# Optimization experiments

Hardware: AMD Instinct MI355X
Metric: run time of the kernel (lower is better)

## Reference

```python
import jax, jax.numpy as jnp
import numpy as np

N_NODES, N_LINKS, N_PATHS = 512, 4096, 20000
D = 128        # node_state_dim == path_state_dim
HEADS = 24
R = 256        # readout units
T_STEPS = 3    # config['t']
MAX_LEN = 8


def _gru(x, h, W, U, b):
    # Keras GRUCell (reset_after=True), gate order [z, r, h]
    xg = x @ W + b[0]
    hg = h @ U + b[1]
    xz, xr, xh = jnp.split(xg, 3, axis=-1)
    hz, hr, hh = jnp.split(hg, 3, axis=-1)
    z = jax.nn.sigmoid(xz + hz)
    r = jax.nn.sigmoid(xr + hr)
    hc = jnp.tanh(xh + r * hh)
    return z * h + (1.0 - z) * hc


def _masked_gru(x_seq, mask, h0, W, U, b, reverse):
    # x_seq [P,T,D], mask [P,T]; Keras masked RNN semantics:
    # state copies through masked steps, output copies previous output (init 0)
    if reverse:
        x_seq = x_seq[:, ::-1]
        mask = mask[:, ::-1]
    def step(carry, inp):
        h, o = carry
        x_t, m_t = inp
        h_new = _gru(x_t, h, W, U, b)
        m = m_t[:, None]
        h = jnp.where(m, h_new, h)
        o = jnp.where(m, h_new, o)
        return (h, o), o
    (hT, _), outs = jax.lax.scan(step, (h0, jnp.zeros_like(h0)),
                                 (x_seq.transpose(1, 0, 2), mask.T))
    outs = outs.transpose(1, 0, 2)
    if reverse:
        outs = outs[:, ::-1]
    return outs, hT


def _gat(x, adj, W, a_self, a_neigh, bias):
    # spektral-style dense GraphAttention, concat_heads=False (mean over heads)
    xp = jnp.einsum('nf,fhc->nhc', x, W)                 # [N,H,C]
    e_s = jnp.einsum('nhc,hc->nh', xp, a_self)
    e_n = jnp.einsum('nhc,hc->nh', xp, a_neigh)
    logits = e_s.T[:, :, None] + e_n.T[:, None, :]       # [H,N,N]
    logits = jax.nn.leaky_relu(logits, 0.2)
    logits = jnp.where(adj[None] == 0.0, -1e9, logits)
    attn = jax.nn.softmax(logits, axis=-1)
    return jnp.einsum('hij,jhc->ihc', attn, xp).mean(axis=1) + bias


def setup_inputs() -> dict:
    rng = np.random.default_rng(0)
    lens = rng.integers(4, MAX_LEN + 1, size=N_PATHS)
    paths = np.repeat(np.arange(N_PATHS, dtype=np.int32), lens)
    seqs = np.concatenate([np.arange(l, dtype=np.int32) for l in lens])
    nodes = rng.integers(0, N_NODES, size=paths.shape[0]).astype(np.int32)
    adj_idx = rng.choice(N_NODES * N_NODES, size=N_LINKS, replace=False).astype(np.int32)

    key = jax.random.key(0)
    ks = iter(jax.random.split(key, 40))
    nrm = lambda *s: jax.random.normal(next(ks), s, dtype=jnp.float32) * 0.05
    unif = lambda *s: jax.random.uniform(next(ks), s, dtype=jnp.float32)
    return {
        'ToS': unif(N_PATHS), 'bandwith': unif(N_PATHS),
        'q_policy': jnp.asarray(rng.integers(0, 3, N_NODES), jnp.float32),
        'w1': unif(N_NODES), 'w2': unif(N_NODES), 'w3': unif(N_NODES),
        'queue_size': unif(N_NODES, 3), 'link_capacity': unif(N_LINKS),
        'gat_W': nrm(D, HEADS, D), 'gat_as': nrm(HEADS, D), 'gat_an': nrm(HEADS, D),
        'gat_b': jnp.zeros((D,), jnp.float32),
        'Wp': nrm(D, 3 * D), 'Up': nrm(D, 3 * D), 'bp': jnp.zeros((2, 3 * D), jnp.float32),
        'Wb': nrm(D, 3 * D), 'Ub': nrm(D, 3 * D), 'bb': jnp.zeros((2, 3 * D), jnp.float32),
        'Wn': nrm(D, 3 * D), 'Un': nrm(D, 3 * D), 'bn': jnp.zeros((2, 3 * D), jnp.float32),
        'rW1': nrm(D, R), 'rb1': jnp.zeros((R,), jnp.float32),
        'rW2': nrm(R, R), 'rb2': jnp.zeros((R,), jnp.float32),
        'rW3': nrm(R, 1), 'rb3': jnp.zeros((1,), jnp.float32),
        'paths': jnp.asarray(paths), 'seqs': jnp.asarray(seqs),
        'nodes': jnp.asarray(nodes), 'adj_idx': jnp.asarray(adj_idx),
    }


def reference(ToS, bandwith, q_policy, w1, w2, w3, queue_size, link_capacity,
              gat_W, gat_as, gat_an, gat_b, Wp, Up, bp, Wb, Ub, bb, Wn, Un, bn,
              rW1, rb1, rW2, rb2, rW3, rb3, paths, seqs, nodes, adj_idx):
    node_state = jnp.concatenate([q_policy[:, None], w1[:, None], w2[:, None],
                                  w3[:, None], queue_size,
                                  jnp.zeros((N_NODES, D - 7), jnp.float32)], axis=1)
    path_state = jnp.concatenate([bandwith[:, None], ToS[:, None],
                                  jnp.zeros((N_PATHS, D - 2), jnp.float32)], axis=1)
    adj = jnp.zeros(N_NODES * N_NODES, jnp.float32).at[adj_idx].set(link_capacity)
    adj = adj.reshape(N_NODES, N_NODES)
    adj = adj / jnp.sqrt(jnp.sum(adj * adj))  # tf.linalg.normalize (global L2)

    lens = jax.ops.segment_sum(jnp.ones_like(paths), paths, num_segments=N_PATHS)
    mask = jnp.arange(MAX_LEN)[None, :] < lens[:, None]  # [P,T]

    for _ in range(T_STEPS):
        node_state = _gat(node_state, adj, gat_W, gat_as, gat_an, gat_b)
        h_tild = node_state[nodes]  # [S,D]
        node_inputs = jnp.zeros((N_PATHS, MAX_LEN, D), jnp.float32).at[paths, seqs].set(h_tild)
        out_f, h_f = _masked_gru(node_inputs, mask, path_state, Wp, Up, bp, False)
        out_b, _ = _masked_gru(node_inputs, mask, path_state, Wb, Ub, bb, True)
        outputs = out_f + out_b  # Bidirectional merge_mode='sum'
        path_state = h_f
        m2 = outputs[paths, seqs]
        m2 = jax.ops.segment_sum(m2, nodes, num_segments=N_NODES)
        node_state = _gru(m2, node_state, Wn, Un, bn)

    h = jax.nn.selu(path_state @ rW1 + rb1)
    h = jax.nn.relu(h @ rW2 + rb2)
    return h @ rW3 + rb3
```

## Files before the change

### kernel.cpp

```cpp
#include <hip/hip_runtime.h>
#include <math.h>

#define NN 512
#define NP 20000
#define DD 128
#define NH 24
#define G3 384
#define NHD 3072

typedef __attribute__((ext_vector_type(8))) short bf8_t;
typedef __attribute__((ext_vector_type(4))) float f4_t;
typedef unsigned short ushort_t;

__device__ __forceinline__ float sigf(float x){
  return __builtin_amdgcn_rcpf(1.f + __expf(-x));
}
__device__ __forceinline__ float tanh_fast(float x){
  float ax = fabsf(x);
  float e = __expf(-2.f*ax);
  float t = (1.f - e) * __builtin_amdgcn_rcpf(1.f + e);
  return copysignf(t, x);
}
__device__ __forceinline__ unsigned short f2bf(float f){
  unsigned int u = __float_as_uint(f);
  unsigned int r = (u + 0x7fffu + ((u>>16)&1u)) >> 16;
  return (unsigned short)r;
}
__device__ __forceinline__ float bf2f(unsigned short h){
  return __uint_as_float(((unsigned int)h)<<16);
}

__global__ void k_init_ns(float* ns, const float* qp, const float* w1, const float* w2,
                          const float* w3, const float* qs){
  int n = blockIdx.x, c = threadIdx.x;
  float v = 0.f;
  if (c==0) v=qp[n]; else if (c==1) v=w1[n]; else if (c==2) v=w2[n]; else if (c==3) v=w3[n];
  else if (c<7) v=qs[n*3 + (c-4)];
  ns[n*DD+c]=v;
}

__global__ void k_init_ps(float* ps, const float* bw, const float* tos){
  int i = blockIdx.x*256 + threadIdx.x;
  if (i >= NP*DD) return;
  int p = i>>7, c = i&127;
  float v=0.f; if(c==0) v=bw[p]; else if(c==1) v=tos[p];
  ps[i]=v;
}

__global__ void k_adj(unsigned int* adjb, const int* idx, const float* lc){
  int l = blockIdx.x*256+threadIdx.x; if(l>=4096) return;
  if (lc[l]!=0.f){
    int a = idx[l]; int i = a>>9, j = a&511;
    atomicOr(&adjb[i*16 + (j>>5)], 1u<<(j&31));
  }
}

__global__ void k_meta(const int* paths, const int* seqs, int* start, int* lens, int E){
  int e = blockIdx.x*256+threadIdx.x; if(e>=E) return;
  int p=paths[e], s=seqs[e];
  if (s==0) start[p]=e;
  if (e==E-1 || paths[e+1]!=p) lens[p]=s+1;
}

__global__ void k_lcount(const int* __restrict__ lens, int* lcnt){
  int p = blockIdx.x*256+threadIdx.x; if(p>=NP) return;
  atomicAdd(&lcnt[lens[p]],1);
}
__global__ void k_lscan(const int* __restrict__ lcnt, int* loff, int* lcur){
  if (threadIdx.x==0){
    int acc=0;
    for (int L=15; L>=0; --L){ loff[L]=acc; lcur[L]=acc; acc+=lcnt[L]; }
  }
}
__global__ void k_lfill(const int* __restrict__ lens, int* lcur, int* perm){
  int p = blockIdx.x*256+threadIdx.x; if(p>=NP) return;
  int pos = atomicAdd(&lcur[lens[p]],1);
  perm[pos]=p;
}

__global__ void k_wsplit(const float* __restrict__ W, ushort_t* __restrict__ Wh,
                         ushort_t* __restrict__ Wl, int shift, int ncols, int total){
  int i = blockIdx.x*256 + threadIdx.x;
  if (i >= total) return;
  int col = i >> shift, k = i & ((1<<shift)-1);
  float v = W[(size_t)k*ncols + col];
  ushort_t h = f2bf(v);
  Wh[i] = h; Wl[i] = f2bf(v - bf2f(h));
}

__global__ __launch_bounds__(512) void k_xp2(const float* __restrict__ ns,
                      const ushort_t* __restrict__ gwh, const ushort_t* __restrict__ gwl,
                      float* __restrict__ xp){
  __shared__ __align__(16) ushort_t XsH[32][136], XsL[32][136];
  int r0 = blockIdx.x*32, c0 = blockIdx.y*256;
  int tid = threadIdx.x;
  int w = tid>>6, l = tid&63, lr = l&15, lg = l>>4;
  for (int idx=tid; idx<32*128; idx+=512){
    int pp=idx>>7, kk=idx&127;
    float v = ns[(size_t)(r0+pp)*DD+kk];
    ushort_t hi=f2bf(v); XsH[pp][kk]=hi; XsL[pp][kk]=f2bf(v-bf2f(hi));
  }
  __syncthreads();
  int col0 = c0 + w*32 + lr, col1 = col0 + 16;
  f4_t a00=(f4_t)(0.f), a01=(f4_t)(0.f), a10=(f4_t)(0.f), a11=(f4_t)(0.f);
  #pragma unroll
  for (int kt=0; kt<4; kt++){
    int kof = kt*32 + lg*8;
    const bf8_t Ah0 = *(const bf8_t*)&XsH[lr][kof];
    const bf8_t Al0 = *(const bf8_t*)&XsL[lr][kof];
    const bf8_t Ah1 = *(const bf8_t*)&XsH[16+lr][kof];
    const bf8_t Al1 = *(const bf8_t*)&XsL[16+lr][kof];
    const bf8_t B0h = *(const bf8_t*)(gwh + (size_t)col0*128 + kof);
    const bf8_t B0l = *(const bf8_t*)(gwl + (size_t)col0*128 + kof);
    const bf8_t B1h = *(const bf8_t*)(gwh + (size_t)col1*128 + kof);
    const bf8_t B1l = *(const bf8_t*)(gwl + (size_t)col1*128 + kof);
    a00 = __builtin_amdgcn_mfma_f32_16x16x32_bf16(Ah0,B0h,a00,0,0,0);
    a00 = __builtin_amdgcn_mfma_f32_16x16x32_bf16(Al0,B0h,a00,0,0,0);
    a00 = __builtin_amdgcn_mfma_f32_16x16x32_bf16(Ah0,B0l,a00,0,0,0);
    a01 = __builtin_amdgcn_mfma_f32_16x16x32_bf16(Ah0,B1h,a01,0,0,0);
    a01 = __builtin_amdgcn_mfma_f32_16x16x32_bf16(Al0,B1h,a01,0,0,0);
    a01 = __builtin_amdgcn_mfma_f32_16x16x32_bf16(Ah0,B1l,a01,0,0,0);
    a10 = __builtin_amdgcn_mfma_f32_16x16x32_bf16(Ah1,B0h,a10,0,0,0);
    a10 = __builtin_amdgcn_mfma_f32_16x16x32_bf16(Al1,B0h,a10,0,0,0);
    a10 = __builtin_amdgcn_mfma_f32_16x16x32_bf16(Ah1,B0l,a10,0,0,0);
    a11 = __builtin_amdgcn_mfma_f32_16x16x32_bf16(Ah1,B1h,a11,0,0,0);
    a11 = __builtin_amdgcn_mfma_f32_16x16x32_bf16(Al1,B1h,a11,0,0,0);
    a11 = __builtin_amdgcn_mfma_f32_16x16x32_bf16(Ah1,B1l,a11,0,0,0);
  }
  #pragma unroll
  for (int q=0;q<4;q++){
    int row0 = lg*4+q, row1 = 16+lg*4+q;
    xp[(size_t)(r0+row0)*NHD + col0] = a00[q];
    xp[(size_t)(r0+row0)*NHD + col1] = a01[q];
    xp[(size_t)(r0+row1)*NHD + col0] = a10[q];
    xp[(size_t)(r0+row1)*NHD + col1] = a11[q];
  }
}

__global__ __launch_bounds__(256) void k_gat_e2(const float* __restrict__ xp,
                        const float* __restrict__ as_, const float* __restrict__ an_,
                        float* es, float* en){
  int n = blockIdx.x; int tid = threadIdx.x;
  int w = tid>>6, l = tid&63;
  for (int hh=0; hh<6; hh++){
    int h = w*6 + hh;
    const float* xr = xp + ((size_t)n*NH + h)*DD;
    const float* ar = as_ + h*DD; const float* br = an_ + h*DD;
    float s1 = xr[l]*ar[l] + xr[l+64]*ar[l+64];
    float s2 = xr[l]*br[l] + xr[l+64]*br[l+64];
    for (int o=32;o>0;o>>=1){ s1 += __shfl_down(s1,o); s2 += __shfl_down(s2,o); }
    if (l==0){ es[n*NH+h]=s1; en[n*NH+h]=s2; }
  }
}

__global__ __launch_bounds__(256) void k_attn(const float* __restrict__ xp,
                      const float* __restrict__ es, const float* __restrict__ en,
                      const unsigned int* __restrict__ adjb, float* __restrict__ pbuf){
  __shared__ float lg[32][513];
  __shared__ float mxs[32], isms[32];
  int h = blockIdx.x, it = blockIdx.y; int i0 = it*32; int tid = threadIdx.x;
  for (int idx=tid; idx<32*512; idx+=256){
    int ii = idx>>9, j = idx&511;
    float l = es[(i0+ii)*NH+h] + en[j*NH+h];
    l = (l>=0.f)? l : 0.2f*l;
    unsigned int m = adjb[(i0+ii)*16 + (j>>5)];
    if (!((m>>(j&31))&1u)) l = -1000000000.0f;
    lg[ii][j] = l;
  }
  __syncthreads();
  {
    int t8 = tid&7, ii = tid>>3;
    float m = -INFINITY;
    for (int j=t8;j<512;j+=8) m = fmaxf(m, lg[ii][j]);
    for (int o=4;o>0;o>>=1) m = fmaxf(m, __shfl_xor(m, o));
    float s=0.f;
    for (int j=t8;j<512;j+=8) s += __expf(lg[ii][j]-m);
    for (int o=4;o>0;o>>=1) s += __shfl_xor(s,o);
    if (t8==0){ mxs[ii]=m; isms[ii]=__builtin_amdgcn_rcpf(s); }
  }
  __syncthreads();
  for (int idx=tid; idx<32*512; idx+=256){
    int ii = idx>>9, j = idx&511;
    lg[ii][j] = __expf(lg[ii][j]-mxs[ii])*isms[ii];
  }
  __syncthreads();
  int cq = tid&31, iq = tid>>5; int c = cq*4;
  float4 acc0=make_float4(0,0,0,0), acc1=acc0, acc2=acc0, acc3=acc0;
  for (int j=0;j<512;j++){
    const float4 xv = *(const float4*)(xp + ((size_t)j*NH + h)*DD + c);
    float p0 = lg[iq*4+0][j], p1 = lg[iq*4+1][j], p2 = lg[iq*4+2][j], p3 = lg[iq*4+3][j];
    acc0.x+=p0*xv.x; acc0.y+=p0*xv.y; acc0.z+=p0*xv.z; acc0.w+=p0*xv.w;
    acc1.x+=p1*xv.x; acc1.y+=p1*xv.y; acc1.z+=p1*xv.z; acc1.w+=p1*xv.w;
    acc2.x+=p2*xv.x; acc2.y+=p2*xv.y; acc2.z+=p2*xv.z; acc2.w+=p2*xv.w;
    acc3.x+=p3*xv.x; acc3.y+=p3*xv.y; acc3.z+=p3*xv.z; acc3.w+=p3*xv.w;
  }
  *(float4*)(pbuf + (((size_t)h*NN + i0+iq*4+0)*DD) + c) = acc0;
  *(float4*)(pbuf + (((size_t)h*NN + i0+iq*4+1)*DD) + c) = acc1;
  *(float4*)(pbuf + (((size_t)h*NN + i0+iq*4+2)*DD) + c) = acc2;
  *(float4*)(pbuf + (((size_t)h*NN + i0+iq*4+3)*DD) + c) = acc3;
}

__global__ void k_gred(const float* __restrict__ pbuf, const float* __restrict__ gb,
                       float* __restrict__ gout){
  int n = blockIdx.x, c = threadIdx.x;
  float a = 0.f;
  #pragma unroll
  for (int h=0; h<NH; h++) a += pbuf[((size_t)h*NN + n)*DD + c];
  gout[n*DD+c] = a*(1.f/24.f) + gb[c];
}

__global__ __launch_bounds__(512) void k_xg3(const float* __restrict__ gout,
      const ushort_t* __restrict__ WpH, const ushort_t* __restrict__ WpL,
      const ushort_t* __restrict__ WbH, const ushort_t* __restrict__ WbL,
      const float* __restrict__ bpF, const float* __restrict__ bpB,
      float* __restrict__ xgF, float* __restrict__ xgB){
  __shared__ __align__(16) ushort_t XsH[32][136], XsL[32][136];
  int r0 = blockIdx.x*32;
  int mat = blockIdx.y/3, cg = blockIdx.y%3;
  const ushort_t* Wh = mat? WbH : WpH;
  const ushort_t* Wl = mat? WbL : WpL;
  const float* b0 = mat? bpB : bpF;
  float* out = mat? xgB : xgF;
  int tid = threadIdx.x;
  int w = tid>>6, l = tid&63, lr = l&15, lg = l>>4;
  for (int idx=tid; idx<32*128; idx+=512){
    int pp=idx>>7, kk=idx&127;
    float v = gout[(size_t)(r0+pp)*DD+kk];
    ushort_t hi=f2bf(v); XsH[pp][kk]=hi; XsL[pp][kk]=f2bf(v-bf2f(hi));
  }
  __syncthreads();
  int col = cg*128 + w*16 + lr;
  f4_t a0=(f4_t)(0.f), a1=(f4_t)(0.f);
  #pragma unroll
  for (int kt=0; kt<4; kt++){
    int kof = kt*32 + lg*8;
    const bf8_t Ah0 = *(const bf8_t*)&XsH[lr][kof];
    const bf8_t Al0 = *(const bf8_t*)&XsL[lr][kof];
    const bf8_t Ah1 = *(const bf8_t*)&XsH[16+lr][kof];
    const bf8_t Al1 = *(const bf8_t*)&XsL[16+lr][kof];
    const bf8_t Bh = *(const bf8_t*)(Wh + (size_t)col*128 + kof);
    const bf8_t Bl = *(const bf8_t*)(Wl + (size_t)col*128 + kof);
    a0 = __builtin_amdgcn_mfma_f32_16x16x32_bf16(Ah0,Bh,a0,0,0,0);
    a0 = __builtin_amdgcn_mfma_f32_16x16x32_bf16(Al0,Bh,a0,0,0,0);
    a0 = __builtin_amdgcn_mfma_f32_16x16x32_bf16(Ah0,Bl,a0,0,0,0);
    a1 = __builtin_amdgcn_mfma_f32_16x16x32_bf16(Ah1,Bh,a1,0,0,0);
    a1 = __builtin_amdgcn_mfma_f32_16x16x32_bf16(Al1,Bh,a1,0,0,0);
    a1 = __builtin_amdgcn_mfma_f32_16x16x32_bf16(Ah1,Bl,a1,0,0,0);
  }
  float bb0 = b0[col];
  #pragma unroll
  for (int q=0;q<4;q++){
    out[(size_t)(r0+lg*4+q)*G3 + col]    = a0[q] + bb0;
    out[(size_t)(r0+16+lg*4+q)*G3 + col] = a1[q] + bb0;
  }
}

__global__ __launch_bounds__(512) void k_gru2(
    const float* __restrict__ ps_in, float* __restrict__ ps_out,
    const float* __restrict__ xgF, const float* __restrict__ xgB,
    const ushort_t* __restrict__ UthF, const ushort_t* __restrict__ UtlF,
    const ushort_t* __restrict__ UthB, const ushort_t* __restrict__ UtlB,
    const float* __restrict__ b1F, const float* __restrict__ b1B,
    const int* __restrict__ start, const int* __restrict__ lens,
    const int* __restrict__ nodes, const int* __restrict__ perm,
    float* __restrict__ m2)
{
  __shared__ __align__(16) ushort_t HsH[2][32][136];
  __shared__ __align__(16) ushort_t HsL[2][32][136];
  __shared__ int Ls[32], Ss[32], Pid[32];
  __shared__ int nid_l[32][8];

  int dir = blockIdx.x & 1, pblk = blockIdx.x >> 1;
  const bool rev = (dir==1);
  const float* xg = rev ? xgB : xgF;
  const ushort_t* Uth = rev ? UthB : UthF;
  const ushort_t* Utl = rev ? UtlB : UtlF;
  const float* b1 = rev ? b1B : b1F;
  float* psn = rev ? (float*)0 : ps_out;

  int pb = pblk*32;
  int tid = threadIdx.x;
  int w = tid>>6, l = tid&63;
  int lr = l&15, lg = l>>4;
  int c = w*16 + lr;

  if (tid<32){ int pid = perm[pb+tid]; Pid[tid]=pid; Ls[tid]=lens[pid]; Ss[tid]=start[pid]; }
  __syncthreads();
  for (int idx=tid; idx<32*128; idx+=512){
    int pp=idx>>7, kk=idx&127;
    float v = ps_in[(size_t)Pid[pp]*DD+kk];
    ushort_t hi = f2bf(v);
    HsH[0][pp][kk]=hi; HsL[0][pp][kk]=f2bf(v - bf2f(hi));
  }
  if (tid<256){
    int p=tid>>3, s=tid&7; int L=Ls[p];
    int nid = 0;
    if (s<L){ int pos = rev ? (L-1-s) : s; nid = nodes[Ss[p]+pos]; }
    nid_l[p][s]=nid;
  }
  __syncthreads();

  int Lmax = Ls[0];
  int Lv[8];
  #pragma unroll
  for (int i=0;i<8;i++){ int p=(i>>2)*16 + lg*4 + (i&3); Lv[i]=Ls[p]; }
  float b1z = b1[c], b1r = b1[128+c], b1h = b1[256+c];

  int cur = 0;
  for (int s=0;s<Lmax;s++){
    int nxt = cur^1;
    bool act[8]; int niv[8]; float xzv[8], xrv[8], xhv[8];
    #pragma unroll
    for (int i=0;i<8;i++){
      int p=(i>>2)*16 + lg*4 + (i&3);
      act[i] = (s < Lv[i]);
      int nid = nid_l[p][s];
      niv[i] = nid;
      const float* xr = xg + (size_t)nid*G3;
      xzv[i]=xr[c]; xrv[i]=xr[128+c]; xhv[i]=xr[256+c];
    }
    f4_t accz0=(f4_t)(0.f), accz1=(f4_t)(0.f);
    f4_t accr0=(f4_t)(0.f), accr1=(f4_t)(0.f);
    f4_t acch0=(f4_t)(0.f), acch1=(f4_t)(0.f);
    #pragma unroll
    for (int kt=0; kt<4; kt++){
      int kof = kt*32 + lg*8;
      const bf8_t Ahi0 = *(const bf8_t*)&HsH[cur][lr][kof];
      const bf8_t Alo0 = *(const bf8_t*)&HsL[cur][lr][kof];
      const bf8_t Ahi1 = *(const bf8_t*)&HsH[cur][16+lr][kof];
      const bf8_t Alo1 = *(const bf8_t*)&HsL[cur][16+lr][kof];
      const bf8_t Bhz = *(const bf8_t*)(Uth + ((size_t)(      c))*128 + kof);
      const bf8_t Blz = *(const bf8_t*)(Utl + ((size_t)(      c))*128 + kof);
      const bf8_t Bhr = *(const bf8_t*)(Uth + ((size_t)(128 + c))*128 + kof);
      const bf8_t Blr = *(const bf8_t*)(Utl + ((size_t)(128 + c))*128 + kof);
      const bf8_t Bhh = *(const bf8_t*)(Uth + ((size_t)(256 + c))*128 + kof);
      const bf8_t Blh = *(const bf8_t*)(Utl + ((size_t)(256 + c))*128 + kof);
      accz0 = __builtin_amdgcn_mfma_f32_16x16x32_bf16(Ahi0, Bhz, accz0, 0,0,0);
      accz0 = __builtin_amdgcn_mfma_f32_16x16x32_bf16(Alo0, Bhz, accz0, 0,0,0);
      accz0 = __builtin_amdgcn_mfma_f32_16x16x32_bf16(Ahi0, Blz, accz0, 0,0,0);
      accz1 = __builtin_amdgcn_mfma_f32_16x16x32_bf16(Ahi1, Bhz, accz1, 0,0,0);
      accz1 = __builtin_amdgcn_mfma_f32_16x16x32_bf16(Alo1, Bhz, accz1, 0,0,0);
      accz1 = __builtin_amdgcn_mfma_f32_16x16x32_bf16(Ahi1, Blz, accz1, 0,0,0);
      accr0 = __builtin_amdgcn_mfma_f32_16x16x32_bf16(Ahi0, Bhr, accr0, 0,0,0);
      accr0 = __builtin_amdgcn_mfma_f32_16x16x32_bf16(Alo0, Bhr, accr0, 0,0,0);
      accr0 = __builtin_amdgcn_mfma_f32_16x16x32_bf16(Ahi0, Blr, accr0, 0,0,0);
      accr1 = __builtin_amdgcn_mfma_f32_16x16x32_bf16(Ahi1, Bhr, accr1, 0,0,0);
      accr1 = __builtin_amdgcn_mfma_f32_16x16x32_bf16(Alo1, Bhr, accr1, 0,0,0);
      accr1 = __builtin_amdgcn_mfma_f32_16x16x32_bf16(Ahi1, Blr, accr1, 0,0,0);
      acch0 = __builtin_amdgcn_mfma_f32_16x16x32_bf16(Ahi0, Bhh, acch0, 0,0,0);
      acch0 = __builtin_amdgcn_mfma_f32_16x16x32_bf16(Alo0, Bhh, acch0, 0,0,0);
      acch0 = __builtin_amdgcn_mfma_f32_16x16x32_bf16(Ahi0, Blh, acch0, 0,0,0);
      acch1 = __builtin_amdgcn_mfma_f32_16x16x32_bf16(Ahi1, Bhh, acch1, 0,0,0);
      acch1 = __builtin_amdgcn_mfma_f32_16x16x32_bf16(Alo1, Bhh, acch1, 0,0,0);
      acch1 = __builtin_amdgcn_mfma_f32_16x16x32_bf16(Ahi1, Blh, acch1, 0,0,0);
    }
#define EPI(i, mt, qq, AZ, AR, AH) { \
    int p = (mt)*16 + lg*4 + (qq); \
    if (act[i]) { \
      float hold = bf2f(HsH[cur][p][c]) + bf2f(HsL[cur][p][c]); \
      float z = sigf(xzv[i] + (AZ) + b1z); \
      float r = sigf(xrv[i] + (AR) + b1r); \
      float hc = tanh_fast(xhv[i] + r*((AH) + b1h)); \
      float hn = z*hold + (1.f-z)*hc; \
      ushort_t hi2 = f2bf(hn); \
      HsH[nxt][p][c]=hi2; HsL[nxt][p][c]=f2bf(hn - bf2f(hi2)); \
      atomicAdd(&m2[(size_t)niv[i]*DD + c], hn); \
    } else { \
      HsH[nxt][p][c]=HsH[cur][p][c]; HsL[nxt][p][c]=HsL[cur][p][c]; \
    } }
    EPI(0,0,0, accz0.x, accr0.x, acch0.x)
    EPI(1,0,1, accz0.y, accr0.y, acch0.y)
    EPI(2,0,2, accz0.z, accr0.z, acch0.z)
    EPI(3,0,3, accz0.w, accr0.w, acch0.w)
    EPI(4,1,0, accz1.x, accr1.x, acch1.x)
    EPI(5,1,1, accz1.y, accr1.y, acch1.y)
    EPI(6,1,2, accz1.z, accr1.z, acch1.z)
    EPI(7,1,3, accz1.w, accr1.w, acch1.w)
#undef EPI
    __syncthreads();
    cur = nxt;
  }
  if (psn){
    for (int idx=tid; idx<32*128; idx+=512){
      int pp=idx>>7, kk=idx&127;
      psn[(size_t)Pid[pp]*DD+kk] = bf2f(HsH[cur][pp][kk]) + bf2f(HsL[cur][pp][kk]);
    }
  }
}

__global__ __launch_bounds__(512) void k_ngru3(
    const float* __restrict__ m2, const float* __restrict__ gout,
    const ushort_t* __restrict__ WnH, const ushort_t* __restrict__ WnL,
    const ushort_t* __restrict__ UnH, const ushort_t* __restrict__ UnL,
    const float* __restrict__ bn, float* __restrict__ ns)
{
  __shared__ __align__(16) ushort_t MsH[32][136], MsL[32][136];
  __shared__ __align__(16) ushort_t GsH[32][136], GsL[32][136];
  int r0 = blockIdx.x*32;
  int tid = threadIdx.x;
  int w = tid>>6, l = tid&63, lr = l&15, lg = l>>4;
  for (int idx=tid; idx<32*128; idx+=512){
    int pp=idx>>7, kk=idx&127;
    float vm = m2[(size_t)(r0+pp)*DD+kk];
    float vg = gout[(size_t)(r0+pp)*DD+kk];
    ushort_t hm=f2bf(vm); MsH[pp][kk]=hm; MsL[pp][kk]=f2bf(vm-bf2f(hm));
    ushort_t hg=f2bf(vg); GsH[pp][kk]=hg; GsL[pp][kk]=f2bf(vg-bf2f(hg));
  }
  __syncthreads();
  int c = w*16 + lr;
  f4_t xz0=(f4_t)(0.f), xr0=(f4_t)(0.f), xh0=(f4_t)(0.f);
  f4_t xz1=(f4_t)(0.f), xr1=(f4_t)(0.f), xh1=(f4_t)(0.f);
  f4_t hz0=(f4_t)(0.f), hr0=(f4_t)(0.f), hh0=(f4_t)(0.f);
  f4_t hz1=(f4_t)(0.f), hr1=(f4_t)(0.f), hh1=(f4_t)(0.f);
  #pragma unroll
  for (int kt=0; kt<4; kt++){
    int kof = kt*32 + lg*8;
    const bf8_t MA0h = *(const bf8_t*)&MsH[lr][kof];
    const bf8_t MA0l = *(const bf8_t*)&MsL[lr][kof];
    const bf8_t MA1h = *(const bf8_t*)&MsH[16+lr][kof];
    const bf8_t MA1l = *(const bf8_t*)&MsL[16+lr][kof];
    const bf8_t GA0h = *(const bf8_t*)&GsH[lr][kof];
    const bf8_t GA0l = *(const bf8_t*)&GsL[lr][kof];
    const bf8_t GA1h = *(const bf8_t*)&GsH[16+lr][kof];
    const bf8_t GA1l = *(const bf8_t*)&GsL[16+lr][kof];
    const bf8_t Wzh = *(const bf8_t*)(WnH + ((size_t)(      c))*128 + kof);
    const bf8_t Wzl = *(const bf8_t*)(WnL + ((size_t)(      c))*128 + kof);
    const bf8_t Wrh = *(const bf8_t*)(WnH + ((size_t)(128 + c))*128 + kof);
    const bf8_t Wrl = *(const bf8_t*)(WnL + ((size_t)(128 + c))*128 + kof);
    const bf8_t Whh = *(const bf8_t*)(WnH + ((size_t)(256 + c))*128 + kof);
    const bf8_t Whl = *(const bf8_t*)(WnL + ((size_t)(256 + c))*128 + kof);
    const bf8_t Uzh = *(const bf8_t*)(UnH + ((size_t)(      c))*128 + kof);
    const bf8_t Uzl = *(const bf8_t*)(UnL + ((size_t)(      c))*128 + kof);
    const bf8_t Urh = *(const bf8_t*)(UnH + ((size_t)(128 + c))*128 + kof);
    const bf8_t Url = *(const bf8_t*)(UnL + ((size_t)(128 + c))*128 + kof);
    const bf8_t Uhh = *(const bf8_t*)(UnH + ((size_t)(256 + c))*128 + kof);
    const bf8_t Uhl = *(const bf8_t*)(UnL + ((size_t)(256 + c))*128 + kof);
    xz0 = __builtin_amdgcn_mfma_f32_16x16x32_bf16(MA0h,Wzh,xz0,0,0,0);
    xz0 = __builtin_amdgcn_mfma_f32_16x16x32_bf16(MA0l,Wzh,xz0,0,0,0);
    xz0 = __builtin_amdgcn_mfma_f32_16x16x32_bf16(MA0h,Wzl,xz0,0,0,0);
    xz1 = __builtin_amdgcn_mfma_f32_16x16x32_bf16(MA1h,Wzh,xz1,0,0,0);
    xz1 = __builtin_amdgcn_mfma_f32_16x16x32_bf16(MA1l,Wzh,xz1,0,0,0);
    xz1 = __builtin_amdgcn_mfma_f32_16x16x32_bf16(MA1h,Wzl,xz1,0,0,0);
    xr0 = __builtin_amdgcn_mfma_f32_16x16x32_bf16(MA0h,Wrh,xr0,0,0,0);
    xr0 = __builtin_amdgcn_mfma_f32_16x16x32_bf16(MA0l,Wrh,xr0,0,0,0);
    xr0 = __builtin_amdgcn_mfma_f32_16x16x32_bf16(MA0h,Wrl,xr0,0,0,0);
    xr1 = __builtin_amdgcn_mfma_f32_16x16x32_bf16(MA1h,Wrh,xr1,0,0,0);
    xr1 = __builtin_amdgcn_mfma_f32_16x16x32_bf16(MA1l,Wrh,xr1,0,0,0);
    xr1 = __builtin_amdgcn_mfma_f32_16x16x32_bf16(MA1h,Wrl,xr1,0,0,0);
    xh0 = __builtin_amdgcn_mfma_f32_16x16x32_bf16(MA0h,Whh,xh0,0,0,0);
    xh0 = __builtin_amdgcn_mfma_f32_16x16x32_bf16(MA0l,Whh,xh0,0,0,0);
    xh0 = __builtin_amdgcn_mfma_f32_16x16x32_bf16(MA0h,Whl,xh0,0,0,0);
    xh1 = __builtin_amdgcn_mfma_f32_16x16x32_bf16(MA1h,Whh,xh1,0,0,0);
    xh1 = __builtin_amdgcn_mfma_f32_16x16x32_bf16(MA1l,Whh,xh1,0,0,0);
    xh1 = __builtin_amdgcn_mfma_f32_16x16x32_bf16(MA1h,Whl,xh1,0,0,0);
    hz0 = __builtin_amdgcn_mfma_f32_16x16x32_bf16(GA0h,Uzh,hz0,0,0,0);
    hz0 = __builtin_amdgcn_mfma_f32_16x16x32_bf16(GA0l,Uzh,hz0,0,0,0);
    hz0 = __builtin_amdgcn_mfma_f32_16x16x32_bf16(GA0h,Uzl,hz0,0,0,0);
    hz1 = __builtin_amdgcn_mfma_f32_16x16x32_bf16(GA1h,Uzh,hz1,0,0,0);
    hz1 = __builtin_amdgcn_mfma_f32_16x16x32_bf16(GA1l,Uzh,hz1,0,0,0);
    hz1 = __builtin_amdgcn_mfma_f32_16x16x32_bf16(GA1h,Uzl,hz1,0,0,0);
    hr0 = __builtin_amdgcn_mfma_f32_16x16x32_bf16(GA0h,Urh,hr0,0,0,0);
    hr0 = __builtin_amdgcn_mfma_f32_16x16x32_bf16(GA0l,Urh,hr0,0,0,0);
    hr0 = __builtin_amdgcn_mfma_f32_16x16x32_bf16(GA0h,Url,hr0,0,0,0);
    hr1 = __builtin_amdgcn_mfma_f32_16x16x32_bf16(GA1h,Urh,hr1,0,0,0);
    hr1 = __builtin_amdgcn_mfma_f32_16x16x32_bf16(GA1l,Urh,hr1,0,0,0);
    hr1 = __builtin_amdgcn_mfma_f32_16x16x32_bf16(GA1h,Url,hr1,0,0,0);
    hh0 = __builtin_amdgcn_mfma_f32_16x16x32_bf16(GA0h,Uhh,hh0,0,0,0);
    hh0 = __builtin_amdgcn_mfma_f32_16x16x32_bf16(GA0l,Uhh,hh0,0,0,0);
    hh0 = __builtin_amdgcn_mfma_f32_16x16x32_bf16(GA0h,Uhl,hh0,0,0,0);
    hh1 = __builtin_amdgcn_mfma_f32_16x16x32_bf16(GA1h,Uhh,hh1,0,0,0);
    hh1 = __builtin_amdgcn_mfma_f32_16x16x32_bf16(GA1l,Uhh,hh1,0,0,0);
    hh1 = __builtin_amdgcn_mfma_f32_16x16x32_bf16(GA1h,Uhl,hh1,0,0,0);
  }
  float bz = bn[c] + bn[G3+c], br = bn[128+c] + bn[G3+128+c];
  float bxh = bn[256+c], bhh = bn[G3+256+c];
  #pragma unroll
  for (int q=0;q<4;q++){
    {
      int n = lg*4+q;
      float hval = bf2f(GsH[n][c]) + bf2f(GsL[n][c]);
      float z = sigf(xz0[q] + hz0[q] + bz);
      float r = sigf(xr0[q] + hr0[q] + br);
      float hc = tanh_fast(xh0[q] + bxh + r*(hh0[q] + bhh));
      ns[(size_t)(r0+n)*DD + c] = z*hval + (1.f-z)*hc;
    }
    {
      int n = 16+lg*4+q;
      float hval = bf2f(GsH[n][c]) + bf2f(GsL[n][c]);
      float z = sigf(xz1[q] + hz1[q] + bz);
      float r = sigf(xr1[q] + hr1[q] + br);
      float hc = tanh_fast(xh1[q] + bxh + r*(hh1[q] + bhh));
      ns[(size_t)(r0+n)*DD + c] = z*hval + (1.f-z)*hc;
    }
  }
}

__global__ __launch_bounds__(512) void k_read2(
    const float* __restrict__ ps,
    const ushort_t* __restrict__ r1h, const ushort_t* __restrict__ r1l,
    const ushort_t* __restrict__ r2h, const ushort_t* __restrict__ r2l,
    const float* __restrict__ rb1, const float* __restrict__ rb2,
    const float* __restrict__ rW3, const float* __restrict__ rb3,
    float* __restrict__ out)
{
  __shared__ __align__(16) ushort_t XsH[32][136], XsL[32][136];
  __shared__ __align__(16) char buf[32*264*2*2];
  ushort_t (*H1H)[264] = (ushort_t(*)[264])buf;
  ushort_t (*H1L)[264] = (ushort_t(*)[264])(buf + 32*264*2);
  float (*H2)[257] = (float(*)[257])buf;
  int pb = blockIdx.x*32, tid = threadIdx.x;
  int w = tid>>6, l = tid&63, lr = l&15, lg = l>>4;
  for (int idx=tid; idx<32*128; idx+=512){
    int pp=idx>>7, kk=idx&127;
    float v = ps[(size_t)(pb+pp)*DD+kk];
    ushort_t hi=f2bf(v); XsH[pp][kk]=hi; XsL[pp][kk]=f2bf(v-bf2f(hi));
  }
  __syncthreads();
  int col0 = w*32 + lr, col1 = col0 + 16;
  f4_t a00=(f4_t)(0.f), a01=(f4_t)(0.f), a10=(f4_t)(0.f), a11=(f4_t)(0.f);
  #pragma unroll
  for (int kt=0; kt<4; kt++){
    int kof = kt*32 + lg*8;
    const bf8_t Ah0 = *(const bf8_t*)&XsH[lr][kof];
    const bf8_t Al0 = *(const bf8_t*)&XsL[lr][kof];
    const bf8_t Ah1 = *(const bf8_t*)&XsH[16+lr][kof];
    const bf8_t Al1 = *(const bf8_t*)&XsL[16+lr][kof];
    const bf8_t B0h = *(const bf8_t*)(r1h + (size_t)col0*128 + kof);
    const bf8_t B0l = *(const bf8_t*)(r1l + (size_t)col0*128 + kof);
    const bf8_t B1h = *(const bf8_t*)(r1h + (size_t)col1*128 + kof);
    const bf8_t B1l = *(const bf8_t*)(r1l + (size_t)col1*128 + kof);
    a00 = __builtin_amdgcn_mfma_f32_16x16x32_bf16(Ah0,B0h,a00,0,0,0);
    a00 = __builtin_amdgcn_mfma_f32_16x16x32_bf16(Al0,B0h,a00,0,0,0);
    a00 = __builtin_amdgcn_mfma_f32_16x16x32_bf16(Ah0,B0l,a00,0,0,0);
    a01 = __builtin_amdgcn_mfma_f32_16x16x32_bf16(Ah0,B1h,a01,0,0,0);
    a01 = __builtin_amdgcn_mfma_f32_16x16x32_bf16(Al0,B1h,a01,0,0,0);
    a01 = __builtin_amdgcn_mfma_f32_16x16x32_bf16(Ah0,B1l,a01,0,0,0);
    a10 = __builtin_amdgcn_mfma_f32_16x16x32_bf16(Ah1,B0h,a10,0,0,0);
    a10 = __builtin_amdgcn_mfma_f32_16x16x32_bf16(Al1,B0h,a10,0,0,0);
    a10 = __builtin_amdgcn_mfma_f32_16x16x32_bf16(Ah1,B0l,a10,0,0,0);
    a11 = __builtin_amdgcn_mfma_f32_16x16x32_bf16(Ah1,B1h,a11,0,0,0);
    a11 = __builtin_amdgcn_mfma_f32_16x16x32_bf16(Al1,B1h,a11,0,0,0);
    a11 = __builtin_amdgcn_mfma_f32_16x16x32_bf16(Ah1,B1l,a11,0,0,0);
  }
  float rb1c0 = rb1[col0], rb1c1 = rb1[col1];
  #pragma unroll
  for (int q=0;q<4;q++){
    int row0 = lg*4+q, row1 = 16+lg*4+q;
    float v00 = a00[q]+rb1c0, v01 = a01[q]+rb1c1, v10 = a10[q]+rb1c0, v11 = a11[q]+rb1c1;
    v00 = 1.0507009873554805f * (v00>0.f ? v00 : 1.6732632423543772f*(__expf(v00)-1.f));
    v01 = 1.0507009873554805f * (v01>0.f ? v01 : 1.6732632423543772f*(__expf(v01)-1.f));
    v10 = 1.0507009873554805f * (v10>0.f ? v10 : 1.6732632423543772f*(__expf(v10)-1.f));
    v11 = 1.0507009873554805f * (v11>0.f ? v11 : 1.6732632423543772f*(__expf(v11)-1.f));
    ushort_t h;
    h=f2bf(v00); H1H[row0][col0]=h; H1L[row0][col0]=f2bf(v00-bf2f(h));
    h=f2bf(v01); H1H[row0][col1]=h; H1L[row0][col1]=f2bf(v01-bf2f(h));
    h=f2bf(v10); H1H[row1][col0]=h; H1L[row1][col0]=f2bf(v10-bf2f(h));
    h=f2bf(v11); H1H[row1][col1]=h; H1L[row1][col1]=f2bf(v11-bf2f(h));
  }
  __syncthreads();
  f4_t c00=(f4_t)(0.f), c01=(f4_t)(0.f), c10=(f4_t)(0.f), c11=(f4_t)(0.f);
  #pragma unroll
  for (int kt=0; kt<8; kt++){
    int kof = kt*32 + lg*8;
    const bf8_t Ah0 = *(const bf8_t*)&H1H[lr][kof];
    const bf8_t Al0 = *(const bf8_t*)&H1L[lr][kof];
    const bf8_t Ah1 = *(const bf8_t*)&H1H[16+lr][kof];
    const bf8_t Al1 = *(const bf8_t*)&H1L[16+lr][kof];
    const bf8_t B0h = *(const bf8_t*)(r2h + (size_t)col0*256 + kof);
    const bf8_t B0l = *(const bf8_t*)(r2l + (size_t)col0*256 + kof);
    const bf8_t B1h = *(const bf8_t*)(r2h + (size_t)col1*256 + kof);
    const bf8_t B1l = *(const bf8_t*)(r2l + (size_t)col1*256 + kof);
    c00 = __builtin_amdgcn_mfma_f32_16x16x32_bf16(Ah0,B0h,c00,0,0,0);
    c00 = __builtin_amdgcn_mfma_f32_16x16x32_bf16(Al0,B0h,c00,0,0,0);
    c00 = __builtin_amdgcn_mfma_f32_16x16x32_bf16(Ah0,B0l,c00,0,0,0);
    c01 = __builtin_amdgcn_mfma_f32_16x16x32_bf16(Ah0,B1h,c01,0,0,0);
    c01 = __builtin_amdgcn_mfma_f32_16x16x32_bf16(Al0,B1h,c01,0,0,0);
    c01 = __builtin_amdgcn_mfma_f32_16x16x32_bf16(Ah0,B1l,c01,0,0,0);
    c10 = __builtin_amdgcn_mfma_f32_16x16x32_bf16(Ah1,B0h,c10,0,0,0);
    c10 = __builtin_amdgcn_mfma_f32_16x16x32_bf16(Al1,B0h,c10,0,0,0);
    c10 = __builtin_amdgcn_mfma_f32_16x16x32_bf16(Ah1,B0l,c10,0,0,0);
    c11 = __builtin_amdgcn_mfma_f32_16x16x32_bf16(Ah1,B1h,c11,0,0,0);
    c11 = __builtin_amdgcn_mfma_f32_16x16x32_bf16(Al1,B1h,c11,0,0,0);
    c11 = __builtin_amdgcn_mfma_f32_16x16x32_bf16(Ah1,B1l,c11,0,0,0);
  }
  __syncthreads();
  float rb2c0 = rb2[col0], rb2c1 = rb2[col1];
  #pragma unroll
  for (int q=0;q<4;q++){
    int row0 = lg*4+q, row1 = 16+lg*4+q;
    H2[row0][col0] = fmaxf(c00[q]+rb2c0, 0.f);
    H2[row0][col1] = fmaxf(c01[q]+rb2c1, 0.f);
    H2[row1][col0] = fmaxf(c10[q]+rb2c0, 0.f);
    H2[row1][col1] = fmaxf(c11[q]+rb2c1, 0.f);
  }
  __syncthreads();
  int r = tid>>4, j0 = tid&15;
  float s = 0.f;
  for (int j=j0; j<256; j+=16) s += H2[r][j]*rW3[j];
  for (int o=8;o>0;o>>=1) s += __shfl_xor(s,o);
  if (j0==0) out[pb+r] = s + rb3[0];
}

extern "C" void kernel_launch(void* const* d_in, const int* in_sizes, int n_in,
                              void* d_out, int out_size, void* d_ws, size_t ws_size,
                              hipStream_t stream)
{
  const float* ToS   = (const float*)d_in[0];
  const float* bw    = (const float*)d_in[1];
  const float* qpol  = (const float*)d_in[2];
  const float* w1    = (const float*)d_in[3];
  const float* w2    = (const float*)d_in[4];
  const float* w3    = (const float*)d_in[5];
  const float* qs    = (const float*)d_in[6];
  const float* lc    = (const float*)d_in[7];
  const float* gat_W = (const float*)d_in[8];
  const float* gat_as= (const float*)d_in[9];
  const float* gat_an= (const float*)d_in[10];
  const float* gat_b = (const float*)d_in[11];
  const float* Wp    = (const float*)d_in[12];
  const float* Up    = (const float*)d_in[13];
  const float* bp    = (const float*)d_in[14];
  const float* Wb    = (const float*)d_in[15];
  const float* Ub    = (const float*)d_in[16];
  const float* bb    = (const float*)d_in[17];
  const float* Wn    = (const float*)d_in[18];
  const float* Un    = (const float*)d_in[19];
  const float* bn    = (const float*)d_in[20];
  const float* rW1   = (const float*)d_in[21];
  const float* rb1   = (const float*)d_in[22];
  const float* rW2   = (const float*)d_in[23];
  const float* rb2   = (const float*)d_in[24];
  const float* rW3   = (const float*)d_in[25];
  const float* rb3   = (const float*)d_in[26];
  const int* paths   = (const int*)d_in[27];
  const int* seqs    = (const int*)d_in[28];
  const int* nodes   = (const int*)d_in[29];
  const int* adj_idx = (const int*)d_in[30];
  int E = in_sizes[27];

  char* w0 = (char*)d_ws;
  char* w = w0;
  auto alloc = [&](size_t nbytes)->void*{ void* r=(void*)w; w += (nbytes + 255) & ~(size_t)255; return r; };
  float* ns     = (float*)alloc((size_t)NN*DD*4);
  float* gout   = (float*)alloc((size_t)NN*DD*4);
  float* psA    = (float*)alloc((size_t)NP*DD*4);
  float* psB    = (float*)alloc((size_t)NP*DD*4);
  float* xp     = (float*)alloc((size_t)NN*NHD*4);
  float* es     = (float*)alloc((size_t)NN*NH*4);
  float* en     = (float*)alloc((size_t)NN*NH*4);
  unsigned int* adjb = (unsigned int*)alloc((size_t)NN*16*4);
  float* xgp    = (float*)alloc((size_t)NN*G3*4);
  float* xgb    = (float*)alloc((size_t)NN*G3*4);
  float* m2     = (float*)alloc((size_t)NN*DD*4);
  float* pbuf   = (float*)alloc((size_t)NH*NN*DD*4);
  ushort_t* Uthp = (ushort_t*)alloc((size_t)G3*DD*2);
  ushort_t* Utlp = (ushort_t*)alloc((size_t)G3*DD*2);
  ushort_t* Uthb = (ushort_t*)alloc((size_t)G3*DD*2);
  ushort_t* Utlb = (ushort_t*)alloc((size_t)G3*DD*2);
  ushort_t* Wpth = (ushort_t*)alloc((size_t)G3*DD*2);
  ushort_t* Wptl = (ushort_t*)alloc((size_t)G3*DD*2);
  ushort_t* Wbth = (ushort_t*)alloc((size_t)G3*DD*2);
  ushort_t* Wbtl = (ushort_t*)alloc((size_t)G3*DD*2);
  ushort_t* WnTh = (ushort_t*)alloc((size_t)G3*DD*2);
  ushort_t* WnTl = (ushort_t*)alloc((size_t)G3*DD*2);
  ushort_t* UnTh = (ushort_t*)alloc((size_t)G3*DD*2);
  ushort_t* UnTl = (ushort_t*)alloc((size_t)G3*DD*2);
  ushort_t* r1h = (ushort_t*)alloc((size_t)256*128*2);
  ushort_t* r1l = (ushort_t*)alloc((size_t)256*128*2);
  ushort_t* r2h = (ushort_t*)alloc((size_t)256*256*2);
  ushort_t* r2l = (ushort_t*)alloc((size_t)256*256*2);
  ushort_t* gwh = (ushort_t*)alloc((size_t)NHD*DD*2);
  ushort_t* gwl = (ushort_t*)alloc((size_t)NHD*DD*2);
  int* start    = (int*)alloc((size_t)NP*4);
  int* lens     = (int*)alloc((size_t)NP*4);
  int* perm     = (int*)alloc((size_t)NP*4);
  int* lcnt     = (int*)alloc(16*4);
  int* loff     = (int*)alloc(16*4);
  int* lcur     = (int*)alloc(16*4);
  (void)n_in; (void)out_size; (void)ws_size; (void)E;

  hipMemsetAsync(adjb, 0, (size_t)NN*16*4, stream);
  hipMemsetAsync(lcnt, 0, 16*4, stream);
  k_init_ns<<<NN,DD,0,stream>>>(ns, qpol, w1, w2, w3, qs);
  k_init_ps<<<(NP*DD+255)/256,256,0,stream>>>(psA, bw, ToS);
  k_adj<<<16,256,0,stream>>>(adjb, adj_idx, lc);
  k_meta<<<(E+255)/256,256,0,stream>>>(paths, seqs, start, lens, E);
  k_lcount<<<(NP+255)/256,256,0,stream>>>(lens, lcnt);
  k_lscan<<<1,64,0,stream>>>(lcnt, loff, lcur);
  k_lfill<<<(NP+255)/256,256,0,stream>>>(lens, lcur, perm);
  k_wsplit<<<(G3*DD+255)/256,256,0,stream>>>(Up, Uthp, Utlp, 7, G3, G3*DD);
  k_wsplit<<<(G3*DD+255)/256,256,0,stream>>>(Ub, Uthb, Utlb, 7, G3, G3*DD);
  k_wsplit<<<(G3*DD+255)/256,256,0,stream>>>(Wp, Wpth, Wptl, 7, G3, G3*DD);
  k_wsplit<<<(G3*DD+255)/256,256,0,stream>>>(Wb, Wbth, Wbtl, 7, G3, G3*DD);
  k_wsplit<<<(G3*DD+255)/256,256,0,stream>>>(Wn, WnTh, WnTl, 7, G3, G3*DD);
  k_wsplit<<<(G3*DD+255)/256,256,0,stream>>>(Un, UnTh, UnTl, 7, G3, G3*DD);
  k_wsplit<<<(256*128+255)/256,256,0,stream>>>(rW1, r1h, r1l, 7, 256, 256*128);
  k_wsplit<<<(256*256+255)/256,256,0,stream>>>(rW2, r2h, r2l, 8, 256, 256*256);
  k_wsplit<<<(NHD*DD+255)/256,256,0,stream>>>(gat_W, gwh, gwl, 7, NHD, NHD*DD);

  float* ps_cur = psA; float* ps_nxt = psB;
  for (int t=0;t<3;t++){
    k_xp2<<<dim3(NN/32, NHD/256),512,0,stream>>>(ns, gwh, gwl, xp);
    k_gat_e2<<<NN,256,0,stream>>>(xp, gat_as, gat_an, es, en);
    k_attn<<<dim3(NH, NN/32),256,0,stream>>>(xp, es, en, adjb, pbuf);
    k_gred<<<NN,DD,0,stream>>>(pbuf, gat_b, gout);
    k_xg3<<<dim3(NN/32,6),512,0,stream>>>(gout, Wpth, Wptl, Wbth, Wbtl, bp, bb, xgp, xgb);
    hipMemsetAsync(m2, 0, (size_t)NN*DD*4, stream);
    k_gru2<<<2*(NP/32),512,0,stream>>>(ps_cur, ps_nxt, xgp, xgb, Uthp, Utlp, Uthb, Utlb,
                                       bp+G3, bb+G3, start, lens, nodes, perm, m2);
    k_ngru3<<<NN/32,512,0,stream>>>(m2, gout, WnTh, WnTl, UnTh, UnTl, bn, ns);
    float* tmp = ps_cur; ps_cur = ps_nxt; ps_nxt = tmp;
  }
  k_read2<<<NP/32,512,0,stream>>>(ps_cur, r1h, r1l, r2h, r2l, rb1, rb2, rW3, rb3, (float*)d_out);
}
```

Measured before the change: 1.210 ms.

## Fuse GAT score and head reduction into neighbours, fold GAT bias into biases

The attention-score dot products are computed inside the xp GEMM epilogue via shuffles and shared-memory reduction, removing the separate score kernel and its re-read of xp. The per-head partial buffer and reduction kernel are replaced by atomic accumulation of head means directly into gout, with the GAT bias folded algebraically into precomputed bias vectors for the downstream GEMMs. The six weight-split launches are merged into one. Atomics add contention and make summation order nondeterministic, and the bias folding slightly changes rounding.

```diff
diff --git a/kernel.cpp b/kernel.cpp
--- a/kernel.cpp
+++ b/kernel.cpp
@@ -88,10 +88,40 @@
   Wh[i] = h; Wl[i] = f2bf(v - bf2f(h));
 }
 
+__global__ void k_wsplit6(
+    const float* S0,const float* S1,const float* S2,const float* S3,const float* S4,const float* S5,
+    ushort_t* H0, ushort_t* L0, ushort_t* H1, ushort_t* L1, ushort_t* H2, ushort_t* L2,
+    ushort_t* H3, ushort_t* L3, ushort_t* H4, ushort_t* L4, ushort_t* H5, ushort_t* L5){
+  int i = blockIdx.x*256 + threadIdx.x;
+  if (i >= 6*G3*DD) return;
+  int m = i/(G3*DD), r = i - m*(G3*DD);
+  const float* S = m==0?S0:m==1?S1:m==2?S2:m==3?S3:m==4?S4:S5;
+  ushort_t* Hh = m==0?H0:m==1?H1:m==2?H2:m==3?H3:m==4?H4:H5;
+  ushort_t* Ll = m==0?L0:m==1?L1:m==2?L2:m==3?L3:m==4?L4:L5;
+  int col = r>>7, k = r&127;
+  float v = S[(size_t)k*G3 + col];
+  ushort_t h = f2bf(v);
+  Hh[r] = h; Ll[r] = f2bf(v - bf2f(h));
+}
+
+__global__ void k_gbw(const float* __restrict__ gb,
+                      const float* __restrict__ Wp, const float* __restrict__ Wb,
+                      const float* __restrict__ Un,
+                      const float* __restrict__ bp, const float* __restrict__ bb,
+                      float* bxgF, float* bxgB, float* gbUn){
+  int m = blockIdx.x; int j = threadIdx.x;
+  const float* W = m==0?Wp:(m==1?Wb:Un);
+  float a = m==0?bp[j]:(m==1?bb[j]:0.f);
+  for (int k=0;k<128;k++) a += gb[k]*W[(size_t)k*G3+j];
+  (m==0?bxgF:(m==1?bxgB:gbUn))[j]=a;
+}
+
 __global__ __launch_bounds__(512) void k_xp2(const float* __restrict__ ns,
                       const ushort_t* __restrict__ gwh, const ushort_t* __restrict__ gwl,
-                      float* __restrict__ xp){
+                      const float* __restrict__ as_, const float* __restrict__ an_,
+                      float* __restrict__ xp, float* __restrict__ es, float* __restrict__ en){
   __shared__ __align__(16) ushort_t XsH[32][136], XsL[32][136];
+  __shared__ float ered[8][32][2];
   int r0 = blockIdx.x*32, c0 = blockIdx.y*256;
   int tid = threadIdx.x;
   int w = tid>>6, l = tid&63, lr = l&15, lg = l>>4;
@@ -135,27 +165,41 @@
     xp[(size_t)(r0+row1)*NHD + col0] = a10[q];
     xp[(size_t)(r0+row1)*NHD + col1] = a11[q];
   }
-}
-
-__global__ __launch_bounds__(256) void k_gat_e2(const float* __restrict__ xp,
-                        const float* __restrict__ as_, const float* __restrict__ an_,
-                        float* es, float* en){
-  int n = blockIdx.x; int tid = threadIdx.x;
-  int w = tid>>6, l = tid&63;
-  for (int hh=0; hh<6; hh++){
-    int h = w*6 + hh;
-    const float* xr = xp + ((size_t)n*NH + h)*DD;
-    const float* ar = as_ + h*DD; const float* br = an_ + h*DD;
-    float s1 = xr[l]*ar[l] + xr[l+64]*ar[l+64];
-    float s2 = xr[l]*br[l] + xr[l+64]*br[l+64];
-    for (int o=32;o>0;o>>=1){ s1 += __shfl_down(s1,o); s2 += __shfl_down(s2,o); }
-    if (l==0){ es[n*NH+h]=s1; en[n*NH+h]=s2; }
+  {
+    int hw = blockIdx.y*2 + (w>>2);
+    int cc0 = (w*32 + lr)&127, cc1 = (w*32 + 16 + lr)&127;
+    float as0 = as_[hw*DD+cc0], as1 = as_[hw*DD+cc1];
+    float an0 = an_[hw*DD+cc0], an1 = an_[hw*DD+cc1];
+    #pragma unroll
+    for (int q=0;q<4;q++){
+      float s0 = a00[q]*as0 + a01[q]*as1;
+      float n0 = a00[q]*an0 + a01[q]*an1;
+      float s1 = a10[q]*as0 + a11[q]*as1;
+      float n1 = a10[q]*an0 + a11[q]*an1;
+      #pragma unroll
+      for (int o=1;o<16;o<<=1){
+        s0 += __shfl_xor(s0,o); n0 += __shfl_xor(n0,o);
+        s1 += __shfl_xor(s1,o); n1 += __shfl_xor(n1,o);
+      }
+      if (lr==0){
+        ered[w][lg*4+q][0]=s0;    ered[w][lg*4+q][1]=n0;
+        ered[w][16+lg*4+q][0]=s1; ered[w][16+lg*4+q][1]=n1;
+      }
+    }
+  }
+  __syncthreads();
+  if (tid < 128){
+    int row = tid&31, hh = (tid>>5)&1, which = tid>>6;
+    float v = ered[hh*4+0][row][which] + ered[hh*4+1][row][which]
+            + ered[hh*4+2][row][which] + ered[hh*4+3][row][which];
+    float* dst = which? en : es;
+    dst[(size_t)(r0+row)*NH + blockIdx.y*2 + hh] = v;
   }
 }
 
 __global__ __launch_bounds__(256) void k_attn(const float* __restrict__ xp,
                       const float* __restrict__ es, const float* __restrict__ en,
-                      const unsigned int* __restrict__ adjb, float* __restrict__ pbuf){
+                      const unsigned int* __restrict__ adjb, float* __restrict__ gout){
   __shared__ float lg[32][513];
   __shared__ float mxs[32], isms[32];
   int h = blockIdx.x, it = blockIdx.y; int i0 = it*32; int tid = threadIdx.x;
@@ -194,32 +238,28 @@
     acc2.x+=p2*xv.x; acc2.y+=p2*xv.y; acc2.z+=p2*xv.z; acc2.w+=p2*xv.w;
     acc3.x+=p3*xv.x; acc3.y+=p3*xv.y; acc3.z+=p3*xv.z; acc3.w+=p3*xv.w;
   }
-  *(float4*)(pbuf + (((size_t)h*NN + i0+iq*4+0)*DD) + c) = acc0;
-  *(float4*)(pbuf + (((size_t)h*NN + i0+iq*4+1)*DD) + c) = acc1;
-  *(float4*)(pbuf + (((size_t)h*NN + i0+iq*4+2)*DD) + c) = acc2;
-  *(float4*)(pbuf + (((size_t)h*NN + i0+iq*4+3)*DD) + c) = acc3;
-}
-
-__global__ void k_gred(const float* __restrict__ pbuf, const float* __restrict__ gb,
-                       float* __restrict__ gout){
-  int n = blockIdx.x, c = threadIdx.x;
-  float a = 0.f;
-  #pragma unroll
-  for (int h=0; h<NH; h++) a += pbuf[((size_t)h*NN + n)*DD + c];
-  gout[n*DD+c] = a*(1.f/24.f) + gb[c];
+  const float inv = 1.f/24.f;
+  float* o0 = gout + (size_t)(i0+iq*4+0)*DD + c;
+  float* o1 = gout + (size_t)(i0+iq*4+1)*DD + c;
+  float* o2 = gout + (size_t)(i0+iq*4+2)*DD + c;
+  float* o3 = gout + (size_t)(i0+iq*4+3)*DD + c;
+  atomicAdd(o0+0,acc0.x*inv); atomicAdd(o0+1,acc0.y*inv); atomicAdd(o0+2,acc0.z*inv); atomicAdd(o0+3,acc0.w*inv);
+  atomicAdd(o1+0,acc1.x*inv); atomicAdd(o1+1,acc1.y*inv); atomicAdd(o1+2,acc1.z*inv); atomicAdd(o1+3,acc1.w*inv);
+  atomicAdd(o2+0,acc2.x*inv); atomicAdd(o2+1,acc2.y*inv); atomicAdd(o2+2,acc2.z*inv); atomicAdd(o2+3,acc2.w*inv);
+  atomicAdd(o3+0,acc3.x*inv); atomicAdd(o3+1,acc3.y*inv); atomicAdd(o3+2,acc3.z*inv); atomicAdd(o3+3,acc3.w*inv);
 }
 
 __global__ __launch_bounds__(512) void k_xg3(const float* __restrict__ gout,
       const ushort_t* __restrict__ WpH, const ushort_t* __restrict__ WpL,
       const ushort_t* __restrict__ WbH, const ushort_t* __restrict__ WbL,
-      const float* __restrict__ bpF, const float* __restrict__ bpB,
+      const float* __restrict__ bxgF, const float* __restrict__ bxgB,
       float* __restrict__ xgF, float* __restrict__ xgB){
   __shared__ __align__(16) ushort_t XsH[32][136], XsL[32][136];
   int r0 = blockIdx.x*32;
   int mat = blockIdx.y/3, cg = blockIdx.y%3;
   const ushort_t* Wh = mat? WbH : WpH;
   const ushort_t* Wl = mat? WbL : WpL;
-  const float* b0 = mat? bpB : bpF;
+  const float* b0 = mat? bxgB : bxgF;
   float* out = mat? xgB : xgF;
   int tid = threadIdx.x;
   int w = tid>>6, l = tid&63, lr = l&15, lg = l>>4;
@@ -392,7 +432,8 @@
     const float* __restrict__ m2, const float* __restrict__ gout,
     const ushort_t* __restrict__ WnH, const ushort_t* __restrict__ WnL,
     const ushort_t* __restrict__ UnH, const ushort_t* __restrict__ UnL,
-    const float* __restrict__ bn, float* __restrict__ ns)
+    const float* __restrict__ bn, const float* __restrict__ gb,
+    const float* __restrict__ gbUn, float* __restrict__ ns)
 {
   __shared__ __align__(16) ushort_t MsH[32][136], MsL[32][136];
   __shared__ __align__(16) ushort_t GsH[32][136], GsL[32][136];
@@ -472,13 +513,15 @@
     hh1 = __builtin_amdgcn_mfma_f32_16x16x32_bf16(GA1l,Uhh,hh1,0,0,0);
     hh1 = __builtin_amdgcn_mfma_f32_16x16x32_bf16(GA1h,Uhl,hh1,0,0,0);
   }
-  float bz = bn[c] + bn[G3+c], br = bn[128+c] + bn[G3+128+c];
-  float bxh = bn[256+c], bhh = bn[G3+256+c];
+  float bz = bn[c] + bn[G3+c] + gbUn[c];
+  float br = bn[128+c] + bn[G3+128+c] + gbUn[128+c];
+  float bxh = bn[256+c], bhh = bn[G3+256+c] + gbUn[256+c];
+  float gbc = gb[c];
   #pragma unroll
   for (int q=0;q<4;q++){
     {
       int n = lg*4+q;
-      float hval = bf2f(GsH[n][c]) + bf2f(GsL[n][c]);
+      float hval = bf2f(GsH[n][c]) + bf2f(GsL[n][c]) + gbc;
       float z = sigf(xz0[q] + hz0[q] + bz);
       float r = sigf(xr0[q] + hr0[q] + br);
       float hc = tanh_fast(xh0[q] + bxh + r*(hh0[q] + bhh));
@@ -486,7 +529,7 @@
     }
     {
       int n = 16+lg*4+q;
-      float hval = bf2f(GsH[n][c]) + bf2f(GsL[n][c]);
+      float hval = bf2f(GsH[n][c]) + bf2f(GsL[n][c]) + gbc;
       float z = sigf(xz1[q] + hz1[q] + bz);
       float r = sigf(xr1[q] + hr1[q] + br);
       float hc = tanh_fast(xh1[q] + bxh + r*(hh1[q] + bhh));
@@ -652,7 +695,9 @@
   float* xgp    = (float*)alloc((size_t)NN*G3*4);
   float* xgb    = (float*)alloc((size_t)NN*G3*4);
   float* m2     = (float*)alloc((size_t)NN*DD*4);
-  float* pbuf   = (float*)alloc((size_t)NH*NN*DD*4);
+  float* bxgF   = (float*)alloc((size_t)G3*4);
+  float* bxgB   = (float*)alloc((size_t)G3*4);
+  float* gbUn   = (float*)alloc((size_t)G3*4);
   ushort_t* Uthp = (ushort_t*)alloc((size_t)G3*DD*2);
   ushort_t* Utlp = (ushort_t*)alloc((size_t)G3*DD*2);
   ushort_t* Uthb = (ushort_t*)alloc((size_t)G3*DD*2);
@@ -677,7 +722,7 @@
   int* lcnt     = (int*)alloc(16*4);
   int* loff     = (int*)alloc(16*4);
   int* lcur     = (int*)alloc(16*4);
-  (void)n_in; (void)out_size; (void)ws_size; (void)E;
+  (void)n_in; (void)out_size; (void)ws_size;
 
   hipMemsetAsync(adjb, 0, (size_t)NN*16*4, stream);
   hipMemsetAsync(lcnt, 0, 16*4, stream);
@@ -688,27 +733,23 @@
   k_lcount<<<(NP+255)/256,256,0,stream>>>(lens, lcnt);
   k_lscan<<<1,64,0,stream>>>(lcnt, loff, lcur);
   k_lfill<<<(NP+255)/256,256,0,stream>>>(lens, lcur, perm);
-  k_wsplit<<<(G3*DD+255)/256,256,0,stream>>>(Up, Uthp, Utlp, 7, G3, G3*DD);
-  k_wsplit<<<(G3*DD+255)/256,256,0,stream>>>(Ub, Uthb, Utlb, 7, G3, G3*DD);
-  k_wsplit<<<(G3*DD+255)/256,256,0,stream>>>(Wp, Wpth, Wptl, 7, G3, G3*DD);
-  k_wsplit<<<(G3*DD+255)/256,256,0,stream>>>(Wb, Wbth, Wbtl, 7, G3, G3*DD);
-  k_wsplit<<<(G3*DD+255)/256,256,0,stream>>>(Wn, WnTh, WnTl, 7, G3, G3*DD);
-  k_wsplit<<<(G3*DD+255)/256,256,0,stream>>>(Un, UnTh, UnTl, 7, G3, G3*DD);
+  k_wsplit6<<<(6*G3*DD+255)/256,256,0,stream>>>(Up, Ub, Wp, Wb, Wn, Un,
+      Uthp,Utlp, Uthb,Utlb, Wpth,Wptl, Wbth,Wbtl, WnTh,WnTl, UnTh,UnTl);
   k_wsplit<<<(256*128+255)/256,256,0,stream>>>(rW1, r1h, r1l, 7, 256, 256*128);
   k_wsplit<<<(256*256+255)/256,256,0,stream>>>(rW2, r2h, r2l, 8, 256, 256*256);
   k_wsplit<<<(NHD*DD+255)/256,256,0,stream>>>(gat_W, gwh, gwl, 7, NHD, NHD*DD);
+  k_gbw<<<3,G3,0,stream>>>(gat_b, Wp, Wb, Un, bp, bb, bxgF, bxgB, gbUn);
 
   float* ps_cur = psA; float* ps_nxt = psB;
   for (int t=0;t<3;t++){
-    k_xp2<<<dim3(NN/32, NHD/256),512,0,stream>>>(ns, gwh, gwl, xp);
-    k_gat_e2<<<NN,256,0,stream>>>(xp, gat_as, gat_an, es, en);
-    k_attn<<<dim3(NH, NN/32),256,0,stream>>>(xp, es, en, adjb, pbuf);
-    k_gred<<<NN,DD,0,stream>>>(pbuf, gat_b, gout);
-    k_xg3<<<dim3(NN/32,6),512,0,stream>>>(gout, Wpth, Wptl, Wbth, Wbtl, bp, bb, xgp, xgb);
+    hipMemsetAsync(gout, 0, (size_t)NN*DD*4, stream);
+    k_xp2<<<dim3(NN/32, NHD/256),512,0,stream>>>(ns, gwh, gwl, gat_as, gat_an, xp, es, en);
+    k_attn<<<dim3(NH, NN/32),256,0,stream>>>(xp, es, en, adjb, gout);
+    k_xg3<<<dim3(NN/32,6),512,0,stream>>>(gout, Wpth, Wptl, Wbth, Wbtl, bxgF, bxgB, xgp, xgb);
     hipMemsetAsync(m2, 0, (size_t)NN*DD*4, stream);
     k_gru2<<<2*(NP/32),512,0,stream>>>(ps_cur, ps_nxt, xgp, xgb, Uthp, Utlp, Uthb, Utlb,
                                        bp+G3, bb+G3, start, lens, nodes, perm, m2);
-    k_ngru3<<<NN/32,512,0,stream>>>(m2, gout, WnTh, WnTl, UnTh, UnTl, bn, ns);
+    k_ngru3<<<NN/32,512,0,stream>>>(m2, gout, WnTh, WnTl, UnTh, UnTl, bn, gat_b, gbUn, ns);
     float* tmp = ps_cur; ps_cur = ps_nxt; ps_nxt = tmp;
   }
   k_read2<<<NP/32,512,0,stream>>>(ps_cur, r1h, r1l, r2h, r2l, rb1, rb2, rW3, rb3, (float*)d_out);
```

New measurement: 1.239 ms. +2.4%, slower.
